# Performance work log

Hardware: AMD Instinct MI355X
Metric: run time of the kernel (lower is better)

## Reference

```python
import jax, jax.numpy as jnp
import numpy as np

V, D, H, L, FF, B, S = 32000, 1024, 16, 4, 4096, 2, 1024
DK = D // H
STD = 0.02


def setup_inputs() -> dict:
    key = jax.random.key(0)
    ks = jax.random.split(key, 9)
    emb = jax.random.normal(ks[0], (V, D), jnp.float32) * STD
    w_qkv = jax.random.normal(ks[1], (L, D, 3 * D), jnp.float32) * STD
    w_o = jax.random.normal(ks[2], (L, D, D), jnp.float32) * STD
    w_gate = jax.random.normal(ks[3], (L, D, FF), jnp.float32) * STD
    w_up = jax.random.normal(ks[4], (L, D, FF), jnp.float32) * STD
    w_down = jax.random.normal(ks[5], (L, FF, D), jnp.float32) * STD
    norm1_w = jnp.ones((L, D), jnp.float32)
    norm2_w = jnp.ones((L, D), jnp.float32)
    final_norm_w = jnp.ones((D,), jnp.float32)
    input_ids = jax.random.randint(ks[6], (B, S), 0, V, dtype=jnp.int32)
    return dict(input_ids=input_ids, emb=emb, w_qkv=w_qkv, w_o=w_o,
                norm1_w=norm1_w, norm2_w=norm2_w,
                w_gate=w_gate, w_up=w_up, w_down=w_down,
                final_norm_w=final_norm_w)


def _rms(x, w, eps=1e-8):
    return w * x / jnp.sqrt(jnp.mean(x * x, axis=-1, keepdims=True) + eps)


def _rope_factor(seq_len, dk):
    # original: x_rope = x*cos + x*sin with cos/sin of shape [S, dk/2]
    # (duplicated along the feature dim to make the broadcast well-defined)
    pos = jnp.arange(seq_len, dtype=jnp.float32)
    freqs = jnp.exp(jnp.arange(0, dk, 2, dtype=jnp.float32) * (-jnp.log(10000.0) / dk))
    ang = pos[:, None] * freqs[None, :]                     # [S, dk/2]
    c = jnp.cos(ang); s = jnp.sin(ang)
    return jnp.concatenate([c, c], -1) + jnp.concatenate([s, s], -1)  # [S, dk]


def reference(input_ids, emb, w_qkv, w_o, norm1_w, norm2_w, w_gate, w_up, w_down, final_norm_w):
    b, s = input_ids.shape
    d = emb.shape[1]
    x = emb[input_ids] * jnp.sqrt(jnp.float32(d))           # [B,S,D]
    rope = _rope_factor(s, DK)                              # [S,DK]
    causal = jnp.tril(jnp.ones((s, s), bool))
    scale = 1.0 / jnp.sqrt(jnp.float32(DK))

    def block(x, p):
        wqkv, wo, n1, n2, wg, wu, wd = p
        nx = _rms(x, n1)
        qkv = (nx @ wqkv).reshape(b, s, 3, H, DK).transpose(2, 0, 3, 1, 4)  # [3,B,H,S,DK]
        q, k, v = qkv[0], qkv[1], qkv[2]
        q = q * rope
        k = k * rope
        scores = jnp.einsum('bhsd,bhtd->bhst', q, k) * scale
        scores = jnp.where(causal, scores, jnp.float32(-1e9))
        attn = jax.nn.softmax(scores, axis=-1)
        o = jnp.einsum('bhst,bhtd->bhsd', attn, v)
        o = o.transpose(0, 2, 1, 3).reshape(b, s, d)
        x = x + o @ wo
        nx = _rms(x, n2)
        ff = (jax.nn.silu(nx @ wg) * (nx @ wu)) @ wd
        return x + ff, None

    x, _ = jax.lax.scan(block, x, (w_qkv, w_o, norm1_w, norm2_w, w_gate, w_up, w_down))
    x = _rms(x, final_norm_w)
    logits = x @ emb.T                                      # tied lm_head
    return logits
```

## Files before the change

kernel.cpp:

```cpp
#include <hip/hip_runtime.h>
#include <hip/hip_bf16.h>
#include <math.h>

#define B_ 2
#define S_ 1024
#define D_ 1024
#define H_ 16
#define DK_ 64
#define L_ 4
#define FF_ 4096
#define V_ 32000
#define NT (B_*S_)

typedef __attribute__((ext_vector_type(8))) short short8v;
typedef __attribute__((ext_vector_type(4))) float floatx4;
typedef __hip_bfloat16 bf16;

__device__ inline float b2f(unsigned short u) {
  unsigned v = ((unsigned)u) << 16;
  float f; __builtin_memcpy(&f, &v, 4); return f;
}
__device__ inline unsigned short f2bu(float f) {
  bf16 h = __float2bfloat16(f);
  unsigned short u; __builtin_memcpy(&u, &h, 2); return u;
}

__global__ __launch_bounds__(256) void k_embed(const int* __restrict__ ids,
    const float* __restrict__ emb, float* __restrict__ x) {
  int i = blockIdx.x*256 + threadIdx.x;
  if (i >= NT*D_) return;
  int tok = i >> 10;
  int d = i & 1023;
  x[i] = emb[(size_t)ids[tok]*D_ + d] * 32.0f;
}

__global__ __launch_bounds__(256) void k_rms(const float* __restrict__ x,
    const float* __restrict__ w, bf16* __restrict__ o) {
  int row = blockIdx.x;
  const float* xr = x + (size_t)row*D_;
  float s = 0.f;
  for (int d = threadIdx.x; d < D_; d += 256) { float v = xr[d]; s += v*v; }
  for (int off = 32; off; off >>= 1) s += __shfl_down(s, off);
  __shared__ float red[4];
  __shared__ float inv_s;
  int wid = threadIdx.x >> 6;
  if ((threadIdx.x & 63) == 0) red[wid] = s;
  __syncthreads();
  if (threadIdx.x == 0) {
    float t = red[0]+red[1]+red[2]+red[3];
    inv_s = 1.0f / sqrtf(t * (1.0f/D_) + 1e-8f);
  }
  __syncthreads();
  float inv = inv_s;
  bf16* orow = o + (size_t)row*D_;
  for (int d = threadIdx.x; d < D_; d += 256) orow[d] = __float2bfloat16(w[d]*xr[d]*inv);
}

__global__ __launch_bounds__(256) void k_transpose_cast(const float* __restrict__ src0,
    bf16* __restrict__ dst0, int K, int N, size_t src_stride, size_t dst_stride) {
  const float* src = src0 + blockIdx.z * src_stride;
  bf16* dst = dst0 + blockIdx.z * dst_stride;
  __shared__ float t[64][65];
  int k0 = blockIdx.y*64, n0 = blockIdx.x*64;
  int r  = threadIdx.x >> 4;
  int c4 = (threadIdx.x & 15)*4;
  #pragma unroll
  for (int i = 0; i < 4; ++i) {
    float4 v = *(const float4*)(src + (size_t)(k0 + r + i*16)*N + n0 + c4);
    t[r+i*16][c4] = v.x; t[r+i*16][c4+1] = v.y;
    t[r+i*16][c4+2] = v.z; t[r+i*16][c4+3] = v.w;
  }
  __syncthreads();
  int nn = threadIdx.x >> 2;
  int kc = threadIdx.x & 3;
  #pragma unroll
  for (int i = 0; i < 4; ++i) {
    int kk = kc*4 + i*16;
    ushort4 o;
    o.x = f2bu(t[kk][nn]);   o.y = f2bu(t[kk+1][nn]);
    o.z = f2bu(t[kk+2][nn]); o.w = f2bu(t[kk+3][nn]);
    *(ushort4*)(dst + (size_t)(n0+nn)*K + k0 + kk) = o;
  }
}

__global__ __launch_bounds__(256) void k_cast4(const float* __restrict__ s,
    bf16* __restrict__ d, int n4) {
  int i = blockIdx.x*256 + threadIdx.x;
  if (i >= n4) return;
  float4 v = ((const float4*)s)[i];
  ushort4 o;
  o.x = f2bu(v.x); o.y = f2bu(v.y); o.z = f2bu(v.z); o.w = f2bu(v.w);
  ((ushort4*)d)[i] = o;
}

template<int EPI, bool OUTBF>
__global__ __launch_bounds__(256) void k_mfma_gemm_bt(
    const bf16* __restrict__ A, const bf16* __restrict__ Bt,
    const void* __restrict__ aux, void* __restrict__ Cout,
    int M, int N, int K) {
  const int NM = M >> 7, NN = N >> 7;
  const int wg = blockIdx.x;
  const int grp = wg >> 3, xcd = wg & 7;
  const int mi = grp % NM;
  const int ni = xcd + 8*(grp / NM);
  if (ni >= NN) return;
  const int bm = mi * 128;
  const int bn = ni * 128;

  __shared__ bf16 As[128*32];
  __shared__ bf16 Bs[128*32];
  const int tid  = threadIdx.x;
  const int lane = tid & 63;
  const int wave = tid >> 6;
  const int wm = (wave >> 1) * 64;
  const int wn = (wave & 1) * 64;

  floatx4 acc[4][4] = {};

  for (int k0 = 0; k0 < K; k0 += 32) {
    #pragma unroll
    for (int c = 0; c < 2; ++c) {
      int e = (c*256 + tid) * 8;
      int row = e >> 5, col = e & 31;
      const bf16* ga = A  + (size_t)(bm + row)*K + k0 + col;
      const bf16* gb = Bt + (size_t)(bn + row)*K + k0 + col;
      int ldsoff = (c*256 + wave*64) * 8;
      __builtin_amdgcn_global_load_lds(
        (const __attribute__((address_space(1))) void*)ga,
        (__attribute__((address_space(3))) void*)(As + ldsoff), 16, 0, 0);
      __builtin_amdgcn_global_load_lds(
        (const __attribute__((address_space(1))) void*)gb,
        (__attribute__((address_space(3))) void*)(Bs + ldsoff), 16, 0, 0);
    }
    __syncthreads();
    const int r = lane & 15, kc = lane >> 4;
    short8v a[4], b[4];
    #pragma unroll
    for (int i = 0; i < 4; ++i) {
      a[i] = *(const short8v*)(As + (size_t)(wm + i*16 + r)*32 + kc*8);
      b[i] = *(const short8v*)(Bs + (size_t)(wn + i*16 + r)*32 + kc*8);
    }
    #pragma unroll
    for (int i = 0; i < 4; ++i)
      #pragma unroll
      for (int j = 0; j < 4; ++j)
        acc[i][j] = __builtin_amdgcn_mfma_f32_16x16x32_bf16(a[i], b[j], acc[i][j], 0, 0, 0);
    __syncthreads();
  }

  const int cn = lane & 15, rq = lane >> 4;
  #pragma unroll
  for (int i=0;i<4;i++) {
    #pragma unroll
    for (int j=0;j<4;j++) {
      const int gcol = bn + wn + j*16 + cn;
      float freq = 0.f;
      if constexpr (EPI==2) {
        if (gcol < 2048)
          freq = expf((float)(gcol & 31) * -0.28782313662425574f);
      }
      #pragma unroll
      for (int rr=0; rr<4; ++rr) {
        const int grow = bm + wm + i*16 + rq*4 + rr;
        const size_t off = (size_t)grow*N + gcol;
        float v = acc[i][j][rr];
        if constexpr (EPI==1) v += ((const float*)aux)[off];
        if constexpr (EPI==2) {
          if (gcol < 2048) {
            float sn, cs;
            sincosf((float)(grow & 1023) * freq, &sn, &cs);
            v *= (cs + sn);
          }
        }
        if constexpr (OUTBF) ((bf16*)Cout)[off] = __float2bfloat16(v);
        else                 ((float*)Cout)[off] = v;
      }
    }
  }
}

static inline int remap_grid(int M, int N) {
  int NM = M >> 7, NN = N >> 7;
  int NN8 = (NN + 7) & ~7;
  return NM * NN8;
}

__global__ __launch_bounds__(256) void k_gemm_64(
    const bf16* __restrict__ A, const bf16* __restrict__ Bt,
    const float* __restrict__ res, float* __restrict__ C,
    int M, int N, int K, int lda) {
  const int NN = N >> 7;
  const int nwg = gridDim.x;
  const int id = (blockIdx.x & 7)*(nwg >> 3) + (blockIdx.x >> 3);
  const int mi = id / NN, ni = id % NN;
  const int bm = mi << 6, bn = ni << 7;

  __shared__ bf16 As2[2][64*32];
  __shared__ bf16 Bs2[2][128*32];
  const int tid  = threadIdx.x;
  const int lane = tid & 63;
  const int wave = tid >> 6;
  const int wm = (wave >> 1) * 32;
  const int wn = (wave & 1) * 64;

  floatx4 acc[2][4] = {};
  const int ntk = K >> 5;

  auto stage = [&](int kt, int buf) {
    {
      int row = tid >> 2, col = (tid & 3)*8;
      const bf16* ga = A + (size_t)(bm + row)*lda + kt*32 + col;
      __builtin_amdgcn_global_load_lds(
        (const __attribute__((address_space(1))) void*)ga,
        (__attribute__((address_space(3))) void*)(As2[buf] + wave*512), 16, 0, 0);
    }
    #pragma unroll
    for (int c = 0; c < 2; ++c) {
      int i = c*256 + tid;
      int row = i >> 2, col = (i & 3)*8;
      const bf16* gb = Bt + (size_t)(bn + row)*K + kt*32 + col;
      __builtin_amdgcn_global_load_lds(
        (const __attribute__((address_space(1))) void*)gb,
        (__attribute__((address_space(3))) void*)(Bs2[buf] + (c*256 + wave*64)*8), 16, 0, 0);
    }
  };

  stage(0, 0);
  int buf = 0;
  for (int t = 0; t < ntk; ++t) {
    if (t + 1 < ntk) {
      stage(t + 1, buf ^ 1);
      asm volatile("s_waitcnt vmcnt(3)" ::: "memory");
    } else {
      asm volatile("s_waitcnt vmcnt(0)" ::: "memory");
    }
    __builtin_amdgcn_sched_barrier(0);
    __builtin_amdgcn_s_barrier();
    __builtin_amdgcn_sched_barrier(0);

    const bf16* Ab = As2[buf];
    const bf16* Bb = Bs2[buf];
    const int r = lane & 15, kc = lane >> 4;
    short8v a[2], b[4];
    #pragma unroll
    for (int i = 0; i < 2; ++i)
      a[i] = *(const short8v*)(Ab + (size_t)(wm + i*16 + r)*32 + kc*8);
    #pragma unroll
    for (int j = 0; j < 4; ++j)
      b[j] = *(const short8v*)(Bb + (size_t)(wn + j*16 + r)*32 + kc*8);
    __builtin_amdgcn_s_setprio(1);
    #pragma unroll
    for (int i = 0; i < 2; ++i)
      #pragma unroll
      for (int j = 0; j < 4; ++j)
        acc[i][j] = __builtin_amdgcn_mfma_f32_16x16x32_bf16(a[i], b[j], acc[i][j], 0, 0, 0);
    __builtin_amdgcn_s_setprio(0);

    __builtin_amdgcn_sched_barrier(0);
    __builtin_amdgcn_s_barrier();
    __builtin_amdgcn_sched_barrier(0);
    buf ^= 1;
  }

  const int cn = lane & 15, rq = lane >> 4;
  #pragma unroll
  for (int i = 0; i < 2; ++i) {
    #pragma unroll
    for (int j = 0; j < 4; ++j) {
      #pragma unroll
      for (int rr = 0; rr < 4; ++rr) {
        int grow = bm + wm + i*16 + rq*4 + rr;
        int gcol = bn + wn + j*16 + cn;
        size_t off = (size_t)grow*N + gcol;
        C[off] = acc[i][j][rr] + res[off];
      }
    }
  }
}

template<bool OUTBF>
__global__ __launch_bounds__(512, 2) void k_gemm256(
    const bf16* __restrict__ A, const bf16* __restrict__ Bt,
    void* __restrict__ C, int M, int N, int K) {
  const int NM = M >> 8;
  const int nwg = gridDim.x;
  const int id = (blockIdx.x & 7)*(nwg >> 3) + (blockIdx.x >> 3);
  const int mi = id % NM, ni = id / NM;
  const int bm = mi << 8, bn = ni << 8;

  __shared__ bf16 As3[3][256*32];
  __shared__ bf16 Bs3[3][256*32];

  const int tid  = threadIdx.x;
  const int lane = tid & 63;
  const int wave = tid >> 6;
  const int wr = wave >> 2;
  const int wc = wave & 3;
  const int fr = lane & 15;
  const int kc = lane >> 4;

  floatx4 acc[8][4] = {};
  const int ntk = K >> 5;

  auto stage_chunk = [&](int kt, int slot, int c) {
    const bf16* Ab = A  + (size_t)bm*K + kt*32;
    const bf16* Bb = Bt + (size_t)bn*K + kt*32;
    int i = c*512 + tid;
    int row = i >> 2, sl = i & 3;
    int gcol = (sl ^ ((row >> 1) & 3)) * 8;
    int ldsoff = (c*512 + wave*64) * 8;
    __builtin_amdgcn_global_load_lds(
      (const __attribute__((address_space(1))) void*)(Ab + (size_t)row*K + gcol),
      (__attribute__((address_space(3))) void*)(&As3[slot][ldsoff]), 16, 0, 0);
    __builtin_amdgcn_global_load_lds(
      (const __attribute__((address_space(1))) void*)(Bb + (size_t)row*K + gcol),
      (__attribute__((address_space(3))) void*)(&Bs3[slot][ldsoff]), 16, 0, 0);
  };

  stage_chunk(0, 0, 0); stage_chunk(0, 0, 1);
  if (ntk > 1) { stage_chunk(1, 1, 0); stage_chunk(1, 1, 1); }

  for (int t = 0; t < ntk; ++t) {
    const int cur = t % 3;
    if (t + 1 < ntk) asm volatile("s_waitcnt vmcnt(4)" ::: "memory");
    else             asm volatile("s_waitcnt vmcnt(0)" ::: "memory");
    __builtin_amdgcn_sched_barrier(0);
    __builtin_amdgcn_s_barrier();
    __builtin_amdgcn_sched_barrier(0);

    const bf16* Ab = As3[cur];
    const bf16* Bb = Bs3[cur];

    short8v a0[4], b[4];
    #pragma unroll
    for (int f = 0; f < 4; ++f) {
      int r = wr*128 + f*16 + fr;
      a0[f] = *(const short8v*)(Ab + r*32 + (kc ^ ((r >> 1) & 3))*8);
    }
    #pragma unroll
    for (int f = 0; f < 4; ++f) {
      int r = wc*64 + f*16 + fr;
      b[f] = *(const short8v*)(Bb + r*32 + (kc ^ ((r >> 1) & 3))*8);
    }
    if (t + 2 < ntk) stage_chunk(t + 2, (t + 2) % 3, 0);
    asm volatile("s_waitcnt lgkmcnt(0)" ::: "memory");
    __builtin_amdgcn_sched_barrier(0);
    __builtin_amdgcn_s_setprio(1);
    #pragma unroll
    for (int f = 0; f < 4; ++f)
      #pragma unroll
      for (int j = 0; j < 4; ++j)
        acc[f][j] = __builtin_amdgcn_mfma_f32_16x16x32_bf16(a0[f], b[j], acc[f][j], 0, 0, 0);
    __builtin_amdgcn_s_setprio(0);
    __builtin_amdgcn_sched_barrier(0);
    __builtin_amdgcn_s_barrier();
    __builtin_amdgcn_sched_barrier(0);

    short8v a1[4];
    #pragma unroll
    for (int f = 0; f < 4; ++f) {
      int r = wr*128 + (f + 4)*16 + fr;
      a1[f] = *(const short8v*)(Ab + r*32 + (kc ^ ((r >> 1) & 3))*8);
    }
    if (t + 2 < ntk) stage_chunk(t + 2, (t + 2) % 3, 1);
    asm volatile("s_waitcnt lgkmcnt(0)" ::: "memory");
    __builtin_amdgcn_sched_barrier(0);
    __builtin_amdgcn_s_setprio(1);
    #pragma unroll
    for (int f = 0; f < 4; ++f)
      #pragma unroll
      for (int j = 0; j < 4; ++j)
        acc[f + 4][j] = __builtin_amdgcn_mfma_f32_16x16x32_bf16(a1[f], b[j], acc[f + 4][j], 0, 0, 0);
    __builtin_amdgcn_s_setprio(0);
    __builtin_amdgcn_sched_barrier(0);
    __builtin_amdgcn_s_barrier();
    __builtin_amdgcn_sched_barrier(0);
  }

  const int cn = lane & 15, rq = lane >> 4;
  #pragma unroll
  for (int f = 0; f < 8; ++f) {
    #pragma unroll
    for (int j = 0; j < 4; ++j) {
      #pragma unroll
      for (int rr = 0; rr < 4; ++rr) {
        int row = bm + wr*128 + f*16 + rq*4 + rr;
        int col = bn + wc*64 + j*16 + cn;
        size_t off = (size_t)row*N + col;
        if constexpr (OUTBF) ((bf16*)C)[off] = __float2bfloat16(acc[f][j][rr]);
        else                 ((float*)C)[off] = acc[f][j][rr];
      }
    }
  }
}

__global__ __launch_bounds__(256) void k_silumul_gu(bf16* __restrict__ gu) {
  int i = blockIdx.x*256 + threadIdx.x;
  if (i >= NT*512) return;
  int row = i >> 9;
  int c8 = (i & 511)*8;
  unsigned short* p = (unsigned short*)gu + (size_t)row*8192 + c8;
  short8v g = *(const short8v*)p;
  short8v u = *(const short8v*)(p + 4096);
  short8v o;
  #pragma unroll
  for (int j = 0; j < 8; ++j) {
    float gf = b2f((unsigned short)g[j]);
    float uf = b2f((unsigned short)u[j]);
    o[j] = (short)f2bu(gf / (1.0f + expf(-gf)) * uf);
  }
  *(short8v*)p = o;
}

__global__ __launch_bounds__(256) void k_vtrans(const bf16* __restrict__ qkvb,
    bf16* __restrict__ vtb) {
  const unsigned short* qkv = (const unsigned short*)qkvb;
  unsigned short* vt = (unsigned short*)vtb;
  const int t0 = blockIdx.x*64, h = blockIdx.y, b = blockIdx.z;
  __shared__ unsigned short t[64][72];
  const int tid = threadIdx.x;
  #pragma unroll
  for (int c = 0; c < 2; ++c) {
    int idx = c*256 + tid;
    int s = idx >> 3, d0 = (idx & 7)*8;
    short8v v = *(const short8v*)(qkv + ((size_t)(b*S_ + t0 + s))*3072 + 2048 + h*DK_ + d0);
    #pragma unroll
    for (int j = 0; j < 8; ++j) t[s][d0+j] = (unsigned short)v[j];
  }
  __syncthreads();
  #pragma unroll
  for (int c = 0; c < 2; ++c) {
    int idx = c*256 + tid;
    int d = idx >> 3, tt0 = (idx & 7)*8;
    short8v o;
    #pragma unroll
    for (int j = 0; j < 8; ++j) o[j] = (short)t[tt0+j][d];
    *(short8v*)(vt + ((size_t)((b*H_ + h)*DK_ + d))*1024 + t0 + tt0) = o;
  }
}

__global__ __launch_bounds__(256) void k_fattn(const bf16* __restrict__ qkvb,
    const bf16* __restrict__ vtb, bf16* __restrict__ outb) {
  const unsigned short* qkv = (const unsigned short*)qkvb;
  const unsigned short* vt  = (const unsigned short*)vtb;
  const int qt = 15 - blockIdx.x;
  const int h = blockIdx.y, b = blockIdx.z;
  const int tid = threadIdx.x, lane = tid & 63, w = tid >> 6;
  const int g = lane >> 4, qn = lane & 15;

  __shared__ unsigned short Ks[2*64*64];
  __shared__ unsigned short Vs[2*64*64];
  __shared__ unsigned short Ps[4*16*64];

  const int q0 = qt * 64;
  const int qw0 = q0 + w*16;

  short8v qf[2];
  {
    const unsigned short* qp = qkv + ((size_t)(b*S_ + qw0 + qn))*3072 + h*DK_ + g*8;
    qf[0] = *(const short8v*)qp;
    qf[1] = *(const short8v*)(qp + 32);
  }

  const int trow = w*8 + (lane>>3);
  const int oct = (lane&7) ^ (trow&7);
  auto stageKV = [&](int it, int buf) {
    const int t0 = it*64;
    #pragma unroll
    for (int c = 0; c < 2; ++c) {
      const unsigned short* gk = qkv + ((size_t)(b*S_ + t0 + c*32 + trow))*3072
                                 + 1024 + h*DK_ + oct*8;
      __builtin_amdgcn_global_load_lds(
        (const __attribute__((address_space(1))) void*)gk,
        (__attribute__((address_space(3))) void*)(Ks + buf*4096 + c*2048 + w*512), 16, 0, 0);
      const unsigned short* gv = vt + ((size_t)((b*H_ + h)*DK_ + c*32 + trow))*1024
                                 + t0 + oct*8;
      __builtin_amdgcn_global_load_lds(
        (const __attribute__((address_space(1))) void*)gv,
        (__attribute__((address_space(3))) void*)(Vs + buf*4096 + c*2048 + w*512), 16, 0, 0);
    }
  };

  floatx4 o_acc[4] = {};
  float m_run = -1e30f, l_run = 0.f;

  const int ntile = qt + 1;
  stageKV(0, 0);
  int cur = 0;

  for (int it = 0; it < ntile; ++it) {
    if (it + 1 < ntile) {
      stageKV(it + 1, cur ^ 1);
      asm volatile("s_waitcnt vmcnt(4)" ::: "memory");
    } else {
      asm volatile("s_waitcnt vmcnt(0)" ::: "memory");
    }
    __builtin_amdgcn_sched_barrier(0);
    __builtin_amdgcn_s_barrier();
    __builtin_amdgcn_sched_barrier(0);

    const unsigned short* Kc = Ks + cur*4096;
    const unsigned short* Vc = Vs + cur*4096;

    floatx4 st[4];
    #pragma unroll
    for (int f = 0; f < 4; ++f) {
      st[f] = (floatx4){0.f,0.f,0.f,0.f};
      int t = f*16 + qn;
      #pragma unroll
      for (int ks = 0; ks < 2; ++ks) {
        int slot = ((ks*4 + g) ^ (t&7)) & 7;
        short8v kf = *(const short8v*)(Kc + t*64 + slot*8);
        st[f] = __builtin_amdgcn_mfma_f32_16x16x32_bf16(kf, qf[ks], st[f], 0,0,0);
      }
    }

    const bool diag = (it == qt);
    float sc[4][4];
    #pragma unroll
    for (int f = 0; f < 4; ++f)
      #pragma unroll
      for (int r = 0; r < 4; ++r) {
        float v = st[f][r]*0.125f;
        if (diag) {
          int tl = f*16 + g*4 + r;
          if (tl > w*16 + qn) v = -1e30f;
        }
        sc[f][r] = v;
      }
    float mx = -1e30f;
    #pragma unroll
    for (int f = 0; f < 4; ++f)
      #pragma unroll
      for (int r = 0; r < 4; ++r) mx = fmaxf(mx, sc[f][r]);
    mx = fmaxf(mx, __shfl_xor(mx, 16));
    mx = fmaxf(mx, __shfl_xor(mx, 32));
    float m_new = fmaxf(m_run, mx);
    float corr = __expf(m_run - m_new);
    m_run = m_new;
    float ls = 0.f;
    #pragma unroll
    for (int f = 0; f < 4; ++f)
      #pragma unroll
      for (int r = 0; r < 4; ++r) {
        float p = __expf(sc[f][r] - m_new);
        sc[f][r] = p;
        ls += p;
      }
    ls += __shfl_xor(ls, 16);
    ls += __shfl_xor(ls, 32);
    l_run = l_run*corr + ls;

    unsigned short* Pw = Ps + w*1024;
    #pragma unroll
    for (int f = 0; f < 4; ++f) {
      unsigned int lo = (unsigned int)f2bu(sc[f][0]) | ((unsigned int)f2bu(sc[f][1]) << 16);
      unsigned int hi = (unsigned int)f2bu(sc[f][2]) | ((unsigned int)f2bu(sc[f][3]) << 16);
      int c16 = f*2 + (g>>1);
      int slot = (c16 ^ (qn&7)) & 7;
      *(uint2*)((char*)Pw + qn*128 + slot*16 + (g&1)*8) = make_uint2(lo, hi);
    }

    #pragma unroll
    for (int r = 0; r < 4; ++r) {
      float cr = __shfl(corr, g*4 + r);
      #pragma unroll
      for (int fd = 0; fd < 4; ++fd) o_acc[fd][r] *= cr;
    }

    short8v pf[2];
    #pragma unroll
    for (int ks = 0; ks < 2; ++ks) {
      int slot = ((ks*4 + g) ^ (qn&7)) & 7;
      pf[ks] = *(const short8v*)(Pw + qn*64 + slot*8);
    }
    #pragma unroll
    for (int fd = 0; fd < 4; ++fd) {
      int d = fd*16 + qn;
      #pragma unroll
      for (int ks = 0; ks < 2; ++ks) {
        int slot = ((ks*4 + g) ^ (d & 7)) & 7;
        short8v vf = *(const short8v*)(Vc + d*64 + slot*8);
        o_acc[fd] = __builtin_amdgcn_mfma_f32_16x16x32_bf16(pf[ks], vf, o_acc[fd], 0,0,0);
      }
    }

    __builtin_amdgcn_sched_barrier(0);
    __builtin_amdgcn_s_barrier();
    __builtin_amdgcn_sched_barrier(0);
    cur ^= 1;
  }

  float linv = 1.0f / l_run;
  #pragma unroll
  for (int r = 0; r < 4; ++r) {
    float li = __shfl(linv, g*4 + r);
    int row = qw0 + g*4 + r;
    bf16* op = outb + (size_t)(b*S_ + row)*D_ + h*DK_ + qn;
    #pragma unroll
    for (int fd = 0; fd < 4; ++fd)
      op[fd*16] = __float2bfloat16(o_acc[fd][r] * li);
  }
}

extern "C" void kernel_launch(void* const* d_in, const int* in_sizes, int n_in,
                              void* d_out, int out_size, void* d_ws, size_t ws_size,
                              hipStream_t stream) {
  (void)in_sizes; (void)n_in; (void)out_size; (void)ws_size;
  const int*   ids  = (const int*)d_in[0];
  const float* emb  = (const float*)d_in[1];
  const float* wqkv = (const float*)d_in[2];
  const float* wo   = (const float*)d_in[3];
  const float* n1   = (const float*)d_in[4];
  const float* n2   = (const float*)d_in[5];
  const float* wg   = (const float*)d_in[6];
  const float* wu   = (const float*)d_in[7];
  const float* wd   = (const float*)d_in[8];
  const float* fnw  = (const float*)d_in[9];
  float* out = (float*)d_out;

  char* ws = (char*)d_ws;
  float* x      = (float*)ws;                                   ws += (size_t)NT*D_*4;
  bf16*  nx_bf  = (bf16*)ws;                                    ws += (size_t)NT*D_*2;
  bf16*  att_bf = (bf16*)ws;                                    ws += (size_t)NT*D_*2;
  bf16*  vt_bf  = (bf16*)ws;                                    ws += (size_t)NT*D_*2;
  bf16*  shared = (bf16*)ws;                                    ws += (size_t)NT*8192*2;
  bf16*  emb_bf = (bf16*)ws;                                    ws += (size_t)V_*D_*2;
  bf16*  qkv_bf = shared;
  bf16*  gu     = shared;

  bf16* wsc = (bf16*)d_out;
  bf16* wqkv_t = wsc;
  bf16* wo_t   = wqkv_t + (size_t)L_*3*D_*D_;
  bf16* wgu_t  = wo_t   + (size_t)L_*D_*D_;
  bf16* wd_t   = wgu_t  + (size_t)L_*2*D_*FF_;

  dim3 blk(256);

  {
    dim3 gq(3*D_/64, D_/64, L_);
    k_transpose_cast<<<gq, blk, 0, stream>>>(wqkv, wqkv_t, D_, 3*D_,
        (size_t)D_*3*D_, (size_t)3*D_*D_);
    dim3 go(D_/64, D_/64, L_);
    k_transpose_cast<<<go, blk, 0, stream>>>(wo, wo_t, D_, D_,
        (size_t)D_*D_, (size_t)D_*D_);
    dim3 gg(FF_/64, D_/64, L_);
    k_transpose_cast<<<gg, blk, 0, stream>>>(wg, wgu_t, D_, FF_,
        (size_t)D_*FF_, (size_t)2*D_*FF_);
    k_transpose_cast<<<gg, blk, 0, stream>>>(wu, wgu_t + (size_t)FF_*D_, D_, FF_,
        (size_t)D_*FF_, (size_t)2*D_*FF_);
    dim3 gdn(D_/64, FF_/64, L_);
    k_transpose_cast<<<gdn, blk, 0, stream>>>(wd, wd_t, FF_, D_,
        (size_t)FF_*D_, (size_t)D_*FF_);
  }
  k_cast4<<<(V_*D_/4 + 255)/256, blk, 0, stream>>>(emb, emb_bf, V_*D_/4);

  k_embed<<<(NT*D_+255)/256, blk, 0, stream>>>(ids, emb, x);

  for (int l = 0; l < L_; ++l) {
    k_rms<<<NT, blk, 0, stream>>>(x, n1 + (size_t)l*D_, nx_bf);
    k_mfma_gemm_bt<2,true><<<remap_grid(NT,3*D_), blk, 0, stream>>>(
        nx_bf, wqkv_t + (size_t)l*3*D_*D_, nullptr, qkv_bf, NT, 3*D_, D_);
    dim3 gvt(S_/64, H_, B_);
    k_vtrans<<<gvt, blk, 0, stream>>>(qkv_bf, vt_bf);
    dim3 gattn(16, H_, B_);
    k_fattn<<<gattn, blk, 0, stream>>>(qkv_bf, vt_bf, att_bf);
    k_gemm_64<<<(NT/64)*(D_/128), blk, 0, stream>>>(
        att_bf, wo_t + (size_t)l*D_*D_, x, x, NT, D_, D_, D_);
    k_rms<<<NT, blk, 0, stream>>>(x, n2 + (size_t)l*D_, nx_bf);
    k_gemm256<true><<<(NT/256)*(2*FF_/256), dim3(512), 0, stream>>>(
        nx_bf, wgu_t + (size_t)l*2*D_*FF_, gu, NT, 2*FF_, D_);
    k_silumul_gu<<<(NT*512 + 255)/256, blk, 0, stream>>>(gu);
    k_gemm_64<<<(NT/64)*(D_/128), blk, 0, stream>>>(
        gu, wd_t + (size_t)l*D_*FF_, x, x, NT, D_, FF_, 2*FF_);
  }
  k_rms<<<NT, blk, 0, stream>>>(x, fnw, nx_bf);
  k_gemm256<false><<<(NT/256)*(V_/256), dim3(512), 0, stream>>>(
      nx_bf, emb_bf, out, NT, V_, D_);
}
```

Baseline: 1.269 ms.

## Fuse SiLU-mul into gate/up GEMM epilogue and V transpose into QKV GEMM

Result: slower. 2.248 ms (+77.2%).

```diff
diff --git a/kernel.cpp b/kernel.cpp
--- a/kernel.cpp
+++ b/kernel.cpp
@@ -57,7 +57,8 @@
 }
 
 __global__ __launch_bounds__(256) void k_transpose_cast(const float* __restrict__ src0,
-    bf16* __restrict__ dst0, int K, int N, size_t src_stride, size_t dst_stride) {
+    bf16* __restrict__ dst0, int K, int N, size_t src_stride, size_t dst_stride,
+    int row_mul, int row_off) {
   const float* src = src0 + blockIdx.z * src_stride;
   bf16* dst = dst0 + blockIdx.z * dst_stride;
   __shared__ float t[64][65];
@@ -79,7 +80,7 @@
     ushort4 o;
     o.x = f2bu(t[kk][nn]);   o.y = f2bu(t[kk+1][nn]);
     o.z = f2bu(t[kk+2][nn]); o.w = f2bu(t[kk+3][nn]);
-    *(ushort4*)(dst + (size_t)(n0+nn)*K + k0 + kk) = o;
+    *(ushort4*)(dst + (size_t)((n0+nn)*row_mul + row_off)*K + k0 + kk) = o;
   }
 }
 
@@ -170,10 +171,17 @@
             float sn, cs;
             sincosf((float)(grow & 1023) * freq, &sn, &cs);
             v *= (cs + sn);
+            ((bf16*)Cout)[off] = __float2bfloat16(v);
+          } else {
+            int d = gcol - 2048;
+            int bb = grow >> 10, s = grow & 1023;
+            size_t vi = (((size_t)bb*H_ + (d >> 6))*DK_ + (d & 63))*1024 + s;
+            ((bf16*)aux)[vi] = __float2bfloat16(v);
           }
+        } else {
+          if constexpr (OUTBF) ((bf16*)Cout)[off] = __float2bfloat16(v);
+          else                 ((float*)Cout)[off] = v;
         }
-        if constexpr (OUTBF) ((bf16*)Cout)[off] = __float2bfloat16(v);
-        else                 ((float*)Cout)[off] = v;
       }
     }
   }
@@ -278,7 +286,7 @@
   }
 }
 
-template<bool OUTBF>
+template<bool OUTBF, bool GUPAIR>
 __global__ __launch_bounds__(512, 2) void k_gemm256(
     const bf16* __restrict__ A, const bf16* __restrict__ Bt,
     void* __restrict__ C, int M, int N, int K) {
@@ -386,56 +394,20 @@
       for (int rr = 0; rr < 4; ++rr) {
         int row = bm + wr*128 + f*16 + rq*4 + rr;
         int col = bn + wc*64 + j*16 + cn;
-        size_t off = (size_t)row*N + col;
-        if constexpr (OUTBF) ((bf16*)C)[off] = __float2bfloat16(acc[f][j][rr]);
-        else                 ((float*)C)[off] = acc[f][j][rr];
-      }
-    }
-  }
-}
-
-__global__ __launch_bounds__(256) void k_silumul_gu(bf16* __restrict__ gu) {
-  int i = blockIdx.x*256 + threadIdx.x;
-  if (i >= NT*512) return;
-  int row = i >> 9;
-  int c8 = (i & 511)*8;
-  unsigned short* p = (unsigned short*)gu + (size_t)row*8192 + c8;
-  short8v g = *(const short8v*)p;
-  short8v u = *(const short8v*)(p + 4096);
-  short8v o;
-  #pragma unroll
-  for (int j = 0; j < 8; ++j) {
-    float gf = b2f((unsigned short)g[j]);
-    float uf = b2f((unsigned short)u[j]);
-    o[j] = (short)f2bu(gf / (1.0f + expf(-gf)) * uf);
-  }
-  *(short8v*)p = o;
-}
-
-__global__ __launch_bounds__(256) void k_vtrans(const bf16* __restrict__ qkvb,
-    bf16* __restrict__ vtb) {
-  const unsigned short* qkv = (const unsigned short*)qkvb;
-  unsigned short* vt = (unsigned short*)vtb;
-  const int t0 = blockIdx.x*64, h = blockIdx.y, b = blockIdx.z;
-  __shared__ unsigned short t[64][72];
-  const int tid = threadIdx.x;
-  #pragma unroll
-  for (int c = 0; c < 2; ++c) {
-    int idx = c*256 + tid;
-    int s = idx >> 3, d0 = (idx & 7)*8;
-    short8v v = *(const short8v*)(qkv + ((size_t)(b*S_ + t0 + s))*3072 + 2048 + h*DK_ + d0);
-    #pragma unroll
-    for (int j = 0; j < 8; ++j) t[s][d0+j] = (unsigned short)v[j];
-  }
-  __syncthreads();
-  #pragma unroll
-  for (int c = 0; c < 2; ++c) {
-    int idx = c*256 + tid;
-    int d = idx >> 3, tt0 = (idx & 7)*8;
-    short8v o;
-    #pragma unroll
-    for (int j = 0; j < 8; ++j) o[j] = (short)t[tt0+j][d];
-    *(short8v*)(vt + ((size_t)((b*H_ + h)*DK_ + d))*1024 + t0 + tt0) = o;
+        float v = acc[f][j][rr];
+        if constexpr (GUPAIR) {
+          float p = __shfl_xor(v, 1);
+          if (!(cn & 1)) {
+            float r2 = v / (1.0f + expf(-v)) * p;
+            ((bf16*)C)[(size_t)row*(N >> 1) + (col >> 1)] = __float2bfloat16(r2);
+          }
+        } else {
+          size_t off = (size_t)row*N + col;
+          if constexpr (OUTBF) ((bf16*)C)[off] = __float2bfloat16(v);
+          else                 ((float*)C)[off] = v;
+        }
+      }
+    }
   }
 }
 
@@ -640,18 +612,18 @@
   {
     dim3 gq(3*D_/64, D_/64, L_);
     k_transpose_cast<<<gq, blk, 0, stream>>>(wqkv, wqkv_t, D_, 3*D_,
-        (size_t)D_*3*D_, (size_t)3*D_*D_);
+        (size_t)D_*3*D_, (size_t)3*D_*D_, 1, 0);
     dim3 go(D_/64, D_/64, L_);
     k_transpose_cast<<<go, blk, 0, stream>>>(wo, wo_t, D_, D_,
-        (size_t)D_*D_, (size_t)D_*D_);
+        (size_t)D_*D_, (size_t)D_*D_, 1, 0);
     dim3 gg(FF_/64, D_/64, L_);
     k_transpose_cast<<<gg, blk, 0, stream>>>(wg, wgu_t, D_, FF_,
-        (size_t)D_*FF_, (size_t)2*D_*FF_);
-    k_transpose_cast<<<gg, blk, 0, stream>>>(wu, wgu_t + (size_t)FF_*D_, D_, FF_,
-        (size_t)D_*FF_, (size_t)2*D_*FF_);
+        (size_t)D_*FF_, (size_t)2*D_*FF_, 2, 0);
+    k_transpose_cast<<<gg, blk, 0, stream>>>(wu, wgu_t, D_, FF_,
+        (size_t)D_*FF_, (size_t)2*D_*FF_, 2, 1);
     dim3 gdn(D_/64, FF_/64, L_);
     k_transpose_cast<<<gdn, blk, 0, stream>>>(wd, wd_t, FF_, D_,
-        (size_t)FF_*D_, (size_t)D_*FF_);
+        (size_t)FF_*D_, (size_t)D_*FF_, 1, 0);
   }
   k_cast4<<<(V_*D_/4 + 255)/256, blk, 0, stream>>>(emb, emb_bf, V_*D_/4);
 
@@ -660,21 +632,18 @@
   for (int l = 0; l < L_; ++l) {
     k_rms<<<NT, blk, 0, stream>>>(x, n1 + (size_t)l*D_, nx_bf);
     k_mfma_gemm_bt<2,true><<<remap_grid(NT,3*D_), blk, 0, stream>>>(
-        nx_bf, wqkv_t + (size_t)l*3*D_*D_, nullptr, qkv_bf, NT, 3*D_, D_);
-    dim3 gvt(S_/64, H_, B_);
-    k_vtrans<<<gvt, blk, 0, stream>>>(qkv_bf, vt_bf);
+        nx_bf, wqkv_t + (size_t)l*3*D_*D_, vt_bf, qkv_bf, NT, 3*D_, D_);
     dim3 gattn(16, H_, B_);
     k_fattn<<<gattn, blk, 0, stream>>>(qkv_bf, vt_bf, att_bf);
     k_gemm_64<<<(NT/64)*(D_/128), blk, 0, stream>>>(
         att_bf, wo_t + (size_t)l*D_*D_, x, x, NT, D_, D_, D_);
     k_rms<<<NT, blk, 0, stream>>>(x, n2 + (size_t)l*D_, nx_bf);
-    k_gemm256<true><<<(NT/256)*(2*FF_/256), dim3(512), 0, stream>>>(
+    k_gemm256<true,true><<<(NT/256)*(2*FF_/256), dim3(512), 0, stream>>>(
         nx_bf, wgu_t + (size_t)l*2*D_*FF_, gu, NT, 2*FF_, D_);
-    k_silumul_gu<<<(NT*512 + 255)/256, blk, 0, stream>>>(gu);
     k_gemm_64<<<(NT/64)*(D_/128), blk, 0, stream>>>(
-        gu, wd_t + (size_t)l*D_*FF_, x, x, NT, D_, FF_, 2*FF_);
+        gu, wd_t + (size_t)l*D_*FF_, x, x, NT, D_, FF_, FF_);
   }
   k_rms<<<NT, blk, 0, stream>>>(x, fnw, nx_bf);
-  k_gemm256<false><<<(NT/256)*(V_/256), dim3(512), 0, stream>>>(
+  k_gemm256<false,false><<<(NT/256)*(V_/256), dim3(512), 0, stream>>>(
       nx_bf, emb_bf, out, NT, V_, D_);
 }
```
